# Optimization experiments

Hardware: AMD Instinct MI355X
Metric: run time of the kernel (lower is better)

## Reference

```python
import jax, jax.numpy as jnp
import numpy as np

EPS = 1e-5
LEAK = 0.1
NPOINT = 4096
NSAMPLE = 32


def setup_inputs() -> dict:
    key = jax.random.key(0)
    ks = jax.random.split(key, 6)
    B, N, Cin = 2, 16384, 64
    ch = [Cin + 3, 64, 64, 128]
    xyz = jax.random.normal(ks[0], (B, 3, N), jnp.float32)
    points = jax.random.normal(ks[1], (B, Cin, N), jnp.float32)
    W0 = jax.random.normal(ks[2], (ch[1], ch[0]), jnp.float32) * 0.05
    W1 = jax.random.normal(ks[3], (ch[2], ch[1]), jnp.float32) * 0.05
    W2 = jax.random.normal(ks[4], (ch[3], ch[2]), jnp.float32) * 0.05
    return dict(
        xyz=xyz, points=points, W0=W0, W1=W1, W2=W2,
        g0=jnp.ones((ch[1],), jnp.float32), b0=jnp.zeros((ch[1],), jnp.float32),
        g1=jnp.ones((ch[2],), jnp.float32), b1=jnp.zeros((ch[2],), jnp.float32),
        g2=jnp.ones((ch[3],), jnp.float32), b2=jnp.zeros((ch[3],), jnp.float32),
    )


def _mlp_bn_act(x, W, g, b):
    # 1x1 conv (no bias) + BatchNorm2d (training: batch stats, biased var) + LeakyReLU(0.1)
    x = jnp.einsum('oc,bcsk->bosk', W, x)
    m = jnp.mean(x, axis=(0, 2, 3), keepdims=True)
    v = jnp.mean(jnp.square(x - m), axis=(0, 2, 3), keepdims=True)
    x = (x - m) * jax.lax.rsqrt(v + EPS) * g[None, :, None, None] + b[None, :, None, None]
    return jnp.where(x >= 0, x, LEAK * x)


def reference(xyz, points, W0, W1, W2, g0, b0, g1, b1, g2, b2):
    B, _, N = xyz.shape
    xyz_t = jnp.transpose(xyz, (0, 2, 1))            # [B,N,3]
    new_xyz = xyz[:, :, :NPOINT]                     # [B,3,S]  (use_fps=False path)
    new_xyz_t = jnp.transpose(new_xyz, (0, 2, 1))    # [B,S,3]

    # squared distances [B,S,N]
    d = (jnp.sum(new_xyz_t ** 2, -1)[:, :, None]
         + jnp.sum(xyz_t ** 2, -1)[:, None, :]
         - 2.0 * jnp.einsum('bsc,bnc->bsn', new_xyz_t, xyz_t))
    _, knn_idx = jax.lax.top_k(-d, NSAMPLE)          # [B,S,K] nearest neighbors

    gather = jax.vmap(lambda arr, idx: arr[idx])     # ([N,C],[S,K]) -> [S,K,C]
    neighbor_xyz = gather(xyz_t, knn_idx)            # [B,S,K,3]
    direction = neighbor_xyz - new_xyz_t[:, :, None, :]
    grouped = gather(jnp.transpose(points, (0, 2, 1)), knn_idx)  # [B,S,K,Cin]

    x = jnp.transpose(jnp.concatenate([direction, grouped], -1), (0, 3, 1, 2))  # [B,Cin+3,S,K]
    x = _mlp_bn_act(x, W0, g0, b0)
    x = _mlp_bn_act(x, W1, g1, b1)
    x = _mlp_bn_act(x, W2, g2, b2)
    new_points = jnp.max(x, axis=-1)                 # [B,128,S] max-pool over nsample
    return new_xyz, new_points
```

## Files before the change

### kernel.cpp

```cpp
#include <hip/hip_runtime.h>
#include <hip/hip_bf16.h>
#include <stdint.h>

#define N_ALL   16384
#define NPOINT  4096
#define KNN_K   32
#define BATCH   2
#define P_TOT   (BATCH*NPOINT*KNN_K)
#define P_TOTF  262144.0f
#define EPSV    1e-5f

typedef __attribute__((ext_vector_type(8))) short bf16x8;
typedef __attribute__((ext_vector_type(4))) float f32x4;

__device__ unsigned short g_knn[P_TOT];
__device__ __attribute__((aligned(16))) float g_pxyzn[BATCH*N_ALL*4];
__device__ __attribute__((aligned(16))) short g_ptb[BATCH*N_ALL*64];
__device__ __attribute__((aligned(16))) short g_x0b[(size_t)P_TOT*64];
__device__ __attribute__((aligned(16))) short g_x1b[(size_t)P_TOT*64];
__device__ __attribute__((aligned(16))) short g_x2b[(size_t)P_TOT*128];
__device__ __attribute__((aligned(16))) short g_Wb0[4*3*64*8];
__device__ __attribute__((aligned(16))) short g_Wb1[4*2*64*8];
__device__ __attribute__((aligned(16))) short g_Wb2[8*2*64*8];
__device__ float g_part0[128], g_part1[128], g_part2[256];

__device__ __forceinline__ float b2f(short s) {
  union { unsigned u; float f; } v; v.u = ((unsigned)(unsigned short)s) << 16; return v.f;
}
__device__ __forceinline__ short f2b(float f) {
  union { float f; unsigned u; } v; v.f = f;
  unsigned u = v.u;
  u += 0x7FFFu + ((u >> 16) & 1u);
  return (short)(u >> 16);
}
__device__ __forceinline__ unsigned pkbf(float a, float b) {
  union { __hip_bfloat162 h; unsigned u; } v;
  v.h = __float22bfloat162_rn(make_float2(a, b));
  return v.u;
}
__device__ __forceinline__ unsigned long long bperm64(unsigned long long v, int byteaddr) {
  int lo = __builtin_amdgcn_ds_bpermute(byteaddr, (int)(unsigned)(v & 0xFFFFFFFFULL));
  int hi = __builtin_amdgcn_ds_bpermute(byteaddr, (int)(unsigned)(v >> 32));
  return (((unsigned long long)(unsigned)hi) << 32) | (unsigned)lo;
}
__device__ __forceinline__ unsigned long long u64min(unsigned long long a, unsigned long long b) {
  return a < b ? a : b;
}
__device__ __forceinline__ unsigned long long selstage(unsigned long long v,
                                                       unsigned long long pv, bool mx) {
  bool lt = v < pv;
  return (lt != mx) ? v : pv;
}

__device__ __forceinline__ void knn_merge32(unsigned long long& vL,
                                            unsigned long long& worst,
                                            unsigned& worst_hi, float& wd,
                                            unsigned long long vB, int hl,
                                            int aX1, int aX2, int aX4, int aX8,
                                            int aX16, int aRev, int aW) {
  vB = selstage(vB, bperm64(vB, aX1),  ((hl & 1) != 0) != ((hl & 2) != 0));
  vB = selstage(vB, bperm64(vB, aX2),  ((hl & 2) != 0) != ((hl & 4) != 0));
  vB = selstage(vB, bperm64(vB, aX1),  ((hl & 1) != 0) != ((hl & 4) != 0));
  vB = selstage(vB, bperm64(vB, aX4),  ((hl & 4) != 0) != ((hl & 8) != 0));
  vB = selstage(vB, bperm64(vB, aX2),  ((hl & 2) != 0) != ((hl & 8) != 0));
  vB = selstage(vB, bperm64(vB, aX1),  ((hl & 1) != 0) != ((hl & 8) != 0));
  vB = selstage(vB, bperm64(vB, aX8),  ((hl & 8) != 0) != ((hl & 16) != 0));
  vB = selstage(vB, bperm64(vB, aX4),  ((hl & 4) != 0) != ((hl & 16) != 0));
  vB = selstage(vB, bperm64(vB, aX2),  ((hl & 2) != 0) != ((hl & 16) != 0));
  vB = selstage(vB, bperm64(vB, aX1),  ((hl & 1) != 0) != ((hl & 16) != 0));
  vB = selstage(vB, bperm64(vB, aX16), (hl & 16) != 0);
  vB = selstage(vB, bperm64(vB, aX8),  (hl & 8) != 0);
  vB = selstage(vB, bperm64(vB, aX4),  (hl & 4) != 0);
  vB = selstage(vB, bperm64(vB, aX2),  (hl & 2) != 0);
  vB = selstage(vB, bperm64(vB, aX1),  (hl & 1) != 0);
  vL = u64min(vL, bperm64(vB, aRev));
  vL = selstage(vL, bperm64(vL, aX16), (hl & 16) != 0);
  vL = selstage(vL, bperm64(vL, aX8),  (hl & 8) != 0);
  vL = selstage(vL, bperm64(vL, aX4),  (hl & 4) != 0);
  vL = selstage(vL, bperm64(vL, aX2),  (hl & 2) != 0);
  vL = selstage(vL, bperm64(vL, aX1),  (hl & 1) != 0);
  worst = bperm64(vL, aW);
  worst_hi = (unsigned)(worst >> 32);
  unsigned wh = worst_hi;
  unsigned ub = (wh & 0x80000000u) ? (wh ^ 0x80000000u) : ~wh;
  wd = (wh == 0xFFFFFFFFu) ? __builtin_inff() : __uint_as_float(ub);
}

__global__ __launch_bounds__(256) void k_setup(const float* __restrict__ xyz,
                                               const float* __restrict__ points,
                                               const float* __restrict__ W0,
                                               const float* __restrict__ W1,
                                               const float* __restrict__ W2,
                                               float* __restrict__ out) {
#pragma clang fp contract(off)
  __shared__ float tile[64][65];
  int blk = blockIdx.x;
  int t = threadIdx.x;
  if (blk < 512) {
    int b  = blk >> 8;
    int n0 = (blk & 255) << 6;
#pragma unroll
    for (int r = 0; r < 16; r++) {
      int lin = r * 256 + t;
      int c = lin >> 6, nn = lin & 63;
      tile[c][nn] = points[((size_t)(b * 64 + c)) * N_ALL + n0 + nn];
    }
    __syncthreads();
#pragma unroll
    for (int r = 0; r < 16; r++) {
      int lin = r * 256 + t;
      int nn = lin >> 6, c = lin & 63;
      g_ptb[((size_t)(b * N_ALL + n0 + nn)) * 64 + c] = f2b(tile[c][nn]);
    }
  } else if (blk < 640) {
    int i = (blk - 512) * 256 + t;
    if (i < 24576) {
      int s = i & 4095;
      int c = (i >> 12) % 3;
      int b = i / 12288;
      out[i] = xyz[(b * 3 + c) * N_ALL + s];
    }
    int b = i >> 14, n = i & 16383;
    const float* xb = xyz + b * 3 * N_ALL;
    float x = xb[n], y = xb[N_ALL + n], z = xb[2 * N_ALL + n];
    float4 p; p.x = x; p.y = y; p.z = z; p.w = x * x + y * y + z * z;
    ((float4*)g_pxyzn)[i] = p;
  } else {
    for (int i = t; i < 4 * 3 * 64 * 8; i += 256) {
      int j = i & 7, lane = (i >> 3) & 63, rest = i >> 9;
      int kt = rest % 3, mt = rest / 3;
      int m = 16 * mt + (lane & 15);
      int k = 32 * kt + (lane >> 4) * 8 + j;
      float v = 0.f;
      if (k < 64) v = W0[m * 67 + 3 + k];
      else if (k < 67) v = W0[m * 67 + (k - 64)];
      g_Wb0[i] = f2b(v);
    }
    for (int i = t; i < 4 * 2 * 64 * 8; i += 256) {
      int j = i & 7, lane = (i >> 3) & 63;
      int kt = (i >> 9) & 1, mt = i >> 10;
      int m = 16 * mt + (lane & 15);
      int k = 32 * kt + (lane >> 4) * 8 + j;
      g_Wb1[i] = f2b(W1[m * 64 + k]);
    }
    for (int i = t; i < 8 * 2 * 64 * 8; i += 256) {
      int j = i & 7, lane = (i >> 3) & 63;
      int kt = (i >> 9) & 1, mt = i >> 10;
      int m = 16 * mt + (lane & 15);
      int k = 32 * kt + (lane >> 4) * 8 + j;
      g_Wb2[i] = f2b(W2[m * 64 + k]);
    }
    if (t < 128) { g_part0[t] = 0.f; g_part1[t] = 0.f; }
    g_part2[t] = 0.f;
  }
}

__global__ __launch_bounds__(256, 8) void k_knn() {
#pragma clang fp contract(off)
  __shared__ unsigned long long buf[4][2][64];
  int wv = threadIdx.x >> 6;
  int lane = threadIdx.x & 63;
  int half = lane >> 5;
  int hl = lane & 31;
  int lanebase = lane & 32;
  unsigned long long* bufh = buf[wv][half];

  int qpair = wv >> 1;
  int range = wv & 1;
  int q = blockIdx.x * 4 + qpair * 2 + half;
  int b = q >> 12, s = q & 4095;
  const float4* pb = (const float4*)g_pxyzn + (b << 14);
  float4 qp = pb[s];
  float qx = qp.x, qy = qp.y, qz = qp.z, qn = qp.w;

  int aX1  = (lanebase | (hl ^ 1))  << 2;
  int aX2  = (lanebase | (hl ^ 2))  << 2;
  int aX4  = (lanebase | (hl ^ 4))  << 2;
  int aX8  = (lanebase | (hl ^ 8))  << 2;
  int aX16 = (lanebase | (hl ^ 16)) << 2;
  int aRev = (lanebase | (31 - hl)) << 2;
  int aW   = (lanebase | 31)        << 2;

  unsigned long long vL = ~0ULL;
  unsigned long long worst = ~0ULL;
  unsigned worst_hi = 0xFFFFFFFFu;
  float wd = __builtin_inff();
  int F = 0;

  int base = range << 13;
  for (int n0 = base; n0 < base + 8192; n0 += 128) {
    float4 p0 = pb[n0 + hl];
    float4 p1 = pb[n0 + 32 + hl];
    float4 p2 = pb[n0 + 64 + hl];
    float4 p3 = pb[n0 + 96 + hl];
    float d[4];
    {
      float dt0 = (qx * p0.x + qy * p0.y) + qz * p0.z;
      float dt1 = (qx * p1.x + qy * p1.y) + qz * p1.z;
      float dt2 = (qx * p2.x + qy * p2.y) + qz * p2.z;
      float dt3 = (qx * p3.x + qy * p3.y) + qz * p3.z;
      d[0] = __builtin_fmaf(-2.0f, dt0, qn + p0.w);
      d[1] = __builtin_fmaf(-2.0f, dt1, qn + p1.w);
      d[2] = __builtin_fmaf(-2.0f, dt2, qn + p2.w);
      d[3] = __builtin_fmaf(-2.0f, dt3, qn + p3.w);
    }
    float md = fminf(fminf(d[0], d[1]), fminf(d[2], d[3]));
    if (__ballot(md <= wd)) {
#pragma unroll
      for (int t = 0; t < 4; t++) {
        bool sv = d[t] <= wd;
        unsigned long long bl = __ballot(sv);
        unsigned mb = half ? (unsigned)(bl >> 32) : (unsigned)bl;
        if (sv) {
          unsigned u = __float_as_uint(d[t]);
          u ^= ((unsigned)(((int)u) >> 31)) | 0x80000000u;
          unsigned long long c = (((unsigned long long)u) << 32)
                               | (unsigned)(n0 + 32 * t + hl);
          bufh[F + __popc(mb & ((1u << hl) - 1u))] = c;
        }
        F += __popc(mb);
        if (__ballot(F >= 32)) {
          int take = F >= 32 ? 32 : F;
          unsigned long long vB = (hl < take) ? bufh[hl] : ~0ULL;
          knn_merge32(vL, worst, worst_hi, wd, vB, hl,
                      aX1, aX2, aX4, aX8, aX16, aRev, aW);
          int R = F - take;
          if (hl < R) bufh[hl] = bufh[32 + hl];
          F = R;
        }
      }
    }
  }
  if (__ballot(F > 0)) {
    unsigned long long vB = (hl < F) ? bufh[hl] : ~0ULL;
    knn_merge32(vL, worst, worst_hi, wd, vB, hl, aX1, aX2, aX4, aX8, aX16, aRev, aW);
  }

  bufh[hl] = vL;
  __syncthreads();
  unsigned long long vB = buf[wv ^ 1][half][hl];
  vL = u64min(vL, bperm64(vB, aRev));
  vL = selstage(vL, bperm64(vL, aX16), (hl & 16) != 0);
  vL = selstage(vL, bperm64(vL, aX8),  (hl & 8) != 0);
  vL = selstage(vL, bperm64(vL, aX4),  (hl & 4) != 0);
  vL = selstage(vL, bperm64(vL, aX2),  (hl & 2) != 0);
  vL = selstage(vL, bperm64(vL, aX1),  (hl & 1) != 0);
  if (range == 0)
    g_knn[((size_t)q << 5) | hl] = (unsigned short)(vL & 0xFFFF);
}

__global__ __launch_bounds__(256) void k_l0(const float* __restrict__ xyz) {
  __shared__ short feats[256][104];
  int t = threadIdx.x;
  int p0 = blockIdx.x * 256;
  {
    int p = p0 + t;
    int idx = g_knn[p];
    int s = (p >> 5) & 4095;
    int b = p >> 17;
    const short* src = g_ptb + ((size_t)((b << 14) + idx) << 6);
#pragma unroll
    for (int i = 0; i < 8; i++)
      ((int4*)&feats[t][0])[i] = ((const int4*)src)[i];
    const float* xb = xyz + b * 3 * N_ALL;
    feats[t][64] = f2b(xb[idx] - xb[s]);
    feats[t][65] = f2b(xb[N_ALL + idx] - xb[N_ALL + s]);
    feats[t][66] = f2b(xb[2 * N_ALL + idx] - xb[2 * N_ALL + s]);
#pragma unroll
    for (int c = 67; c < 96; c++) feats[t][c] = 0;
  }
  __syncthreads();
  int lane = t & 63, wv = t >> 6;
  int l15 = lane & 15, quad = lane >> 4;
  bf16x8 A[4][3];
#pragma unroll
  for (int mt = 0; mt < 4; mt++)
#pragma unroll
    for (int kt = 0; kt < 3; kt++)
      A[mt][kt] = *(const bf16x8*)(g_Wb0 + (((mt * 3 + kt) * 64 + lane) << 3));
  f32x4 C[4][4];
#pragma unroll
  for (int mt = 0; mt < 4; mt++)
#pragma unroll
    for (int nt = 0; nt < 4; nt++) C[mt][nt] = 0.f;
#pragma unroll
  for (int kt = 0; kt < 3; kt++)
#pragma unroll
    for (int nt = 0; nt < 4; nt++) {
      bf16x8 B = *(const bf16x8*)(&feats[wv * 64 + nt * 16 + l15][kt * 32 + quad * 8]);
#pragma unroll
      for (int mt = 0; mt < 4; mt++)
        C[mt][nt] = __builtin_amdgcn_mfma_f32_16x16x32_bf16(A[mt][kt], B, C[mt][nt], 0, 0, 0);
    }
#pragma unroll
  for (int mt = 0; mt < 4; mt++)
#pragma unroll
    for (int nt = 0; nt < 4; nt++) {
      int p = p0 + wv * 64 + nt * 16 + l15;
      int c0 = mt * 16 + quad * 4;
      uint2 o;
      o.x = pkbf(C[mt][nt][0], C[mt][nt][1]);
      o.y = pkbf(C[mt][nt][2], C[mt][nt][3]);
      *(uint2*)(g_x0b + ((size_t)p << 6) + c0) = o;
    }
}

__global__ __launch_bounds__(256) void k_l1(const float* __restrict__ g0,
                                            const float* __restrict__ b0) {
  __shared__ float scA[64], shA[64];
  int t = threadIdx.x;
  if (t < 64) {
    float m = g_part0[t] / P_TOTF;
    float v = g_part0[64 + t] / P_TOTF - m * m;
    float sc = g0[t] / sqrtf(v + EPSV);
    scA[t] = sc; shA[t] = b0[t] - m * sc;
  }
  __syncthreads();
  int lane = t & 63, wv = t >> 6;
  int l15 = lane & 15, quad = lane >> 4;
  int p0 = blockIdx.x * 256 + wv * 64;
  float scv[2][8], shv[2][8];
#pragma unroll
  for (int kt = 0; kt < 2; kt++)
#pragma unroll
    for (int j = 0; j < 8; j++) {
      int c = kt * 32 + quad * 8 + j;
      scv[kt][j] = scA[c]; shv[kt][j] = shA[c];
    }
  bf16x8 A[4][2];
#pragma unroll
  for (int mt = 0; mt < 4; mt++)
#pragma unroll
    for (int kt = 0; kt < 2; kt++)
      A[mt][kt] = *(const bf16x8*)(g_Wb1 + (((mt * 2 + kt) * 64 + lane) << 3));
  f32x4 C[4][4];
#pragma unroll
  for (int mt = 0; mt < 4; mt++)
#pragma unroll
    for (int nt = 0; nt < 4; nt++) C[mt][nt] = 0.f;
#pragma unroll
  for (int kt = 0; kt < 2; kt++)
#pragma unroll
    for (int nt = 0; nt < 4; nt++) {
      const short* src = g_x0b + (((size_t)(p0 + nt * 16 + l15)) << 6) + kt * 32 + quad * 8;
      uint4 raw = *(const uint4*)src;
      bf16x8 B;
      unsigned* Bu = (unsigned*)&B;
      unsigned ru[4] = {raw.x, raw.y, raw.z, raw.w};
#pragma unroll
      for (int jj = 0; jj < 4; jj++) {
        float lo = __uint_as_float(ru[jj] << 16);
        float hi = __uint_as_float(ru[jj] & 0xFFFF0000u);
        float a0 = lo * scv[kt][2*jj]   + shv[kt][2*jj];
        float a1 = hi * scv[kt][2*jj+1] + shv[kt][2*jj+1];
        a0 = fmaxf(a0, 0.1f * a0);
        a1 = fmaxf(a1, 0.1f * a1);
        Bu[jj] = pkbf(a0, a1);
      }
#pragma unroll
      for (int mt = 0; mt < 4; mt++)
        C[mt][nt] = __builtin_amdgcn_mfma_f32_16x16x32_bf16(A[mt][kt], B, C[mt][nt], 0, 0, 0);
    }
#pragma unroll
  for (int mt = 0; mt < 4; mt++)
#pragma unroll
    for (int nt = 0; nt < 4; nt++) {
      int p = p0 + nt * 16 + l15;
      int c0 = mt * 16 + quad * 4;
      uint2 o;
      o.x = pkbf(C[mt][nt][0], C[mt][nt][1]);
      o.y = pkbf(C[mt][nt][2], C[mt][nt][3]);
      *(uint2*)(g_x1b + ((size_t)p << 6) + c0) = o;
    }
}

__global__ __launch_bounds__(256) void k_l2(const float* __restrict__ g1,
                                            const float* __restrict__ b1) {
  __shared__ float scA[64], shA[64];
  int t = threadIdx.x;
  if (t < 64) {
    float m = g_part1[t] / P_TOTF;
    float v = g_part1[64 + t] / P_TOTF - m * m;
    float sc = g1[t] / sqrtf(v + EPSV);
    scA[t] = sc; shA[t] = b1[t] - m * sc;
  }
  __syncthreads();
  int lane = t & 63, wv = t >> 6;
  int l15 = lane & 15, quad = lane >> 4;
  int chh = wv & 1;
  int p0 = blockIdx.x * 128 + (wv >> 1) * 64;
  float scv[2][8], shv[2][8];
#pragma unroll
  for (int kt = 0; kt < 2; kt++)
#pragma unroll
    for (int j = 0; j < 8; j++) {
      int c = kt * 32 + quad * 8 + j;
      scv[kt][j] = scA[c]; shv[kt][j] = shA[c];
    }
  bf16x8 A[4][2];
#pragma unroll
  for (int mt = 0; mt < 4; mt++)
#pragma unroll
    for (int kt = 0; kt < 2; kt++)
      A[mt][kt] = *(const bf16x8*)(g_Wb2 + ((((4 * chh + mt) * 2 + kt) * 64 + lane) << 3));
  f32x4 C[4][4];
#pragma unroll
  for (int mt = 0; mt < 4; mt++)
#pragma unroll
    for (int nt = 0; nt < 4; nt++) C[mt][nt] = 0.f;
#pragma unroll
  for (int kt = 0; kt < 2; kt++)
#pragma unroll
    for (int nt = 0; nt < 4; nt++) {
      const short* src = g_x1b + (((size_t)(p0 + nt * 16 + l15)) << 6) + kt * 32 + quad * 8;
      uint4 raw = *(const uint4*)src;
      bf16x8 B;
      unsigned* Bu = (unsigned*)&B;
      unsigned ru[4] = {raw.x, raw.y, raw.z, raw.w};
#pragma unroll
      for (int jj = 0; jj < 4; jj++) {
        float lo = __uint_as_float(ru[jj] << 16);
        float hi = __uint_as_float(ru[jj] & 0xFFFF0000u);
        float a0 = lo * scv[kt][2*jj]   + shv[kt][2*jj];
        float a1 = hi * scv[kt][2*jj+1] + shv[kt][2*jj+1];
        a0 = fmaxf(a0, 0.1f * a0);
        a1 = fmaxf(a1, 0.1f * a1);
        Bu[jj] = pkbf(a0, a1);
      }
#pragma unroll
      for (int mt = 0; mt < 4; mt++)
        C[mt][nt] = __builtin_amdgcn_mfma_f32_16x16x32_bf16(A[mt][kt], B, C[mt][nt], 0, 0, 0);
    }
#pragma unroll
  for (int mt = 0; mt < 4; mt++)
#pragma unroll
    for (int nt = 0; nt < 4; nt++) {
      int p = p0 + nt * 16 + l15;
      int c0 = (4 * chh + mt) * 16 + quad * 4;
      uint2 o;
      o.x = pkbf(C[mt][nt][0], C[mt][nt][1]);
      o.y = pkbf(C[mt][nt][2], C[mt][nt][3]);
      *(uint2*)(g_x2b + ((size_t)p << 7) + c0) = o;
    }
}

__global__ __launch_bounds__(256) void k_red64(const short* __restrict__ x,
                                               float* __restrict__ part) {
  int t = threadIdx.x;
  int cl = t & 31, pr = t >> 5;
  float s0 = 0.f, s1 = 0.f, q0 = 0.f, q1 = 0.f;
  int pbase = blockIdx.x * 1024;
  for (int i = 0; i < 128; i++) {
    int p = pbase + pr + i * 8;
    unsigned d = *(const unsigned*)(x + ((size_t)p << 6) + cl * 2);
    float a = b2f((short)(d & 0xFFFF));
    float b = b2f((short)(d >> 16));
    s0 += a; q0 = fmaf(a, a, q0);
    s1 += b; q1 = fmaf(b, b, q1);
  }
  __shared__ float sm[8][64], sq[8][64];
  sm[pr][cl * 2] = s0; sm[pr][cl * 2 + 1] = s1;
  sq[pr][cl * 2] = q0; sq[pr][cl * 2 + 1] = q1;
  __syncthreads();
  if (t < 64) {
    float S = 0.f, Q = 0.f;
#pragma unroll
    for (int r = 0; r < 8; r++) { S += sm[r][t]; Q += sq[r][t]; }
    atomicAdd(part + t, S); atomicAdd(part + 64 + t, Q);
  }
}

__global__ __launch_bounds__(256) void k_red128(const short* __restrict__ x,
                                                float* __restrict__ part) {
  int t = threadIdx.x;
  int cl = t & 63, pr = t >> 6;
  float s0 = 0.f, s1 = 0.f, q0 = 0.f, q1 = 0.f;
  int pbase = blockIdx.x * 1024;
  for (int i = 0; i < 256; i++) {
    int p = pbase + pr + i * 4;
    unsigned d = *(const unsigned*)(x + ((size_t)p << 7) + cl * 2);
    float a = b2f((short)(d & 0xFFFF));
    float b = b2f((short)(d >> 16));
    s0 += a; q0 = fmaf(a, a, q0);
    s1 += b; q1 = fmaf(b, b, q1);
  }
  __shared__ float sm[4][128], sq[4][128];
  sm[pr][cl * 2] = s0; sm[pr][cl * 2 + 1] = s1;
  sq[pr][cl * 2] = q0; sq[pr][cl * 2 + 1] = q1;
  __syncthreads();
  if (t < 128) {
    float S = 0.f, Q = 0.f;
#pragma unroll
    for (int r = 0; r < 4; r++) { S += sm[r][t]; Q += sq[r][t]; }
    atomicAdd(part + t, S); atomicAdd(part + 128 + t, Q);
  }
}

__global__ __launch_bounds__(256) void k_epi(const float* __restrict__ g2,
                                             const float* __restrict__ b2,
                                             float* __restrict__ out) {
  __shared__ float scA[128], shA[128];
  __shared__ float res[16][132];
  int t = threadIdx.x;
  if (t < 128) {
    float m = g_part2[t] / P_TOTF;
    float v = g_part2[128 + t] / P_TOTF - m * m;
    float sc = g2[t] / sqrtf(v + EPSV);
    scA[t] = sc; shA[t] = b2[t] - m * sc;
  }
  __syncthreads();
  int cp = t & 63, sl = t >> 6;
  int c0 = cp * 2, c1 = c0 + 1;
  float sc0 = scA[c0], sh0 = shA[c0];
  float sc1 = scA[c1], sh1 = shA[c1];
  int sg0 = blockIdx.x * 16;
  for (int it = 0; it < 4; it++) {
    int sgl = sl * 4 + it;
    size_t pbase = ((size_t)(sg0 + sgl)) << 5;
    float mx0 = -3.4e38f, mn0 = 3.4e38f, mx1 = -3.4e38f, mn1 = 3.4e38f;
#pragma unroll
    for (int k = 0; k < 32; k++) {
      unsigned u = *(const unsigned*)(g_x2b + ((pbase + k) << 7) + cp * 2);
      float v0 = __uint_as_float(u << 16);
      float v1 = __uint_as_float(u & 0xFFFF0000u);
      mx0 = fmaxf(mx0, v0); mn0 = fminf(mn0, v0);
      mx1 = fmaxf(mx1, v1); mn1 = fminf(mn1, v1);
    }
    float a0 = (sc0 >= 0.f ? mx0 : mn0) * sc0 + sh0; a0 = fmaxf(a0, 0.1f * a0);
    float a1 = (sc1 >= 0.f ? mx1 : mn1) * sc1 + sh1; a1 = fmaxf(a1, 0.1f * a1);
    res[sgl][c0] = a0; res[sgl][c1] = a1;
  }
  __syncthreads();
  int b = sg0 >> 12, s0 = sg0 & 4095;
#pragma unroll
  for (int w = 0; w < 2; w++) {
    int fidx = t * 2 + w;
    int c = fidx >> 2, qi = fidx & 3;
    float4 o;
    o.x = res[qi * 4 + 0][c];
    o.y = res[qi * 4 + 1][c];
    o.z = res[qi * 4 + 2][c];
    o.w = res[qi * 4 + 3][c];
    *(float4*)(out + 24576 + (((size_t)(b * 128 + c)) << 12) + s0 + qi * 4) = o;
  }
}

extern "C" void kernel_launch(void* const* d_in, const int* in_sizes, int n_in,
                              void* d_out, int out_size, void* d_ws, size_t ws_size,
                              hipStream_t stream) {
  (void)in_sizes; (void)n_in; (void)out_size; (void)d_ws; (void)ws_size;
  const float* xyz    = (const float*)d_in[0];
  const float* points = (const float*)d_in[1];
  const float* W0     = (const float*)d_in[2];
  const float* W1     = (const float*)d_in[3];
  const float* W2     = (const float*)d_in[4];
  const float* g0     = (const float*)d_in[5];
  const float* b0     = (const float*)d_in[6];
  const float* g1     = (const float*)d_in[7];
  const float* b1     = (const float*)d_in[8];
  const float* g2     = (const float*)d_in[9];
  const float* b2     = (const float*)d_in[10];
  float* out = (float*)d_out;

  short *x0b, *x1b, *x2b; float *part0, *part1, *part2;
  hipGetSymbolAddress((void**)&x0b,   HIP_SYMBOL(g_x0b));
  hipGetSymbolAddress((void**)&x1b,   HIP_SYMBOL(g_x1b));
  hipGetSymbolAddress((void**)&x2b,   HIP_SYMBOL(g_x2b));
  hipGetSymbolAddress((void**)&part0, HIP_SYMBOL(g_part0));
  hipGetSymbolAddress((void**)&part1, HIP_SYMBOL(g_part1));
  hipGetSymbolAddress((void**)&part2, HIP_SYMBOL(g_part2));

  hipLaunchKernelGGL(k_setup,  dim3(641),  dim3(256), 0, stream, xyz, points, W0, W1, W2, out);
  hipLaunchKernelGGL(k_knn,    dim3(2048), dim3(256), 0, stream);
  hipLaunchKernelGGL(k_l0,     dim3(1024), dim3(256), 0, stream, xyz);
  hipLaunchKernelGGL(k_red64,  dim3(256),  dim3(256), 0, stream, x0b, part0);
  hipLaunchKernelGGL(k_l1,     dim3(1024), dim3(256), 0, stream, g0, b0);
  hipLaunchKernelGGL(k_red64,  dim3(256),  dim3(256), 0, stream, x1b, part1);
  hipLaunchKernelGGL(k_l2,     dim3(2048), dim3(256), 0, stream, g1, b1);
  hipLaunchKernelGGL(k_red128, dim3(256),  dim3(256), 0, stream, x2b, part2);
  hipLaunchKernelGGL(k_epi,    dim3(512),  dim3(256), 0, stream, g2, b2, out);
}
```

Measured before the change: 321.5 us.

## Fuse per-group max/min pooling into layer-2 stats reduction, vectorize feature padding

The final BN-statistics reduction now walks points group by group and also computes each group's per-channel max and min, writing them to small float buffers. The epilogue then reads these precomputed extrema instead of re-reading the full 128-channel bf16 activation tensor. This removes a second full pass over the largest intermediate, in exchange for small extra buffers and a changed access order in the reduction. Separately, the zero padding and direction features in k_l0 are written with vector stores instead of scalar ones.

```diff
diff --git a/kernel.cpp b/kernel.cpp
--- a/kernel.cpp
+++ b/kernel.cpp
@@ -19,6 +19,8 @@
 __device__ __attribute__((aligned(16))) short g_x0b[(size_t)P_TOT*64];
 __device__ __attribute__((aligned(16))) short g_x1b[(size_t)P_TOT*64];
 __device__ __attribute__((aligned(16))) short g_x2b[(size_t)P_TOT*128];
+__device__ __attribute__((aligned(16))) float g_mx[(size_t)BATCH*NPOINT*128];
+__device__ __attribute__((aligned(16))) float g_mn[(size_t)BATCH*NPOINT*128];
 __device__ __attribute__((aligned(16))) short g_Wb0[4*3*64*8];
 __device__ __attribute__((aligned(16))) short g_Wb1[4*2*64*8];
 __device__ __attribute__((aligned(16))) short g_Wb2[8*2*64*8];
@@ -263,11 +265,17 @@
     for (int i = 0; i < 8; i++)
       ((int4*)&feats[t][0])[i] = ((const int4*)src)[i];
     const float* xb = xyz + b * 3 * N_ALL;
-    feats[t][64] = f2b(xb[idx] - xb[s]);
-    feats[t][65] = f2b(xb[N_ALL + idx] - xb[N_ALL + s]);
-    feats[t][66] = f2b(xb[2 * N_ALL + idx] - xb[2 * N_ALL + s]);
-#pragma unroll
-    for (int c = 67; c < 96; c++) feats[t][c] = 0;
+    int4 z; z.x = 0; z.y = 0; z.z = 0; z.w = 0;
+    *(int4*)&feats[t][64] = z;
+    *(int4*)&feats[t][72] = z;
+    *(int4*)&feats[t][80] = z;
+    *(int4*)&feats[t][88] = z;
+    short4 d3;
+    d3.x = f2b(xb[idx] - xb[s]);
+    d3.y = f2b(xb[N_ALL + idx] - xb[N_ALL + s]);
+    d3.z = f2b(xb[2 * N_ALL + idx] - xb[2 * N_ALL + s]);
+    d3.w = 0;
+    *(short4*)&feats[t][64] = d3;
   }
   __syncthreads();
   int lane = t & 63, wv = t >> 6;
@@ -470,23 +478,34 @@
   }
 }
 
-__global__ __launch_bounds__(256) void k_red128(const short* __restrict__ x,
-                                                float* __restrict__ part) {
-  int t = threadIdx.x;
-  int cl = t & 63, pr = t >> 6;
+__global__ __launch_bounds__(256) void k_red128mx(const short* __restrict__ x,
+                                                  float* __restrict__ part) {
+  int t = threadIdx.x;
+  int cl = t & 63, wv = t >> 6;
   float s0 = 0.f, s1 = 0.f, q0 = 0.f, q1 = 0.f;
-  int pbase = blockIdx.x * 1024;
-  for (int i = 0; i < 256; i++) {
-    int p = pbase + pr + i * 4;
-    unsigned d = *(const unsigned*)(x + ((size_t)p << 7) + cl * 2);
-    float a = b2f((short)(d & 0xFFFF));
-    float b = b2f((short)(d >> 16));
-    s0 += a; q0 = fmaf(a, a, q0);
-    s1 += b; q1 = fmaf(b, b, q1);
+  int g0 = blockIdx.x * 32;
+  for (int it = 0; it < 8; it++) {
+    int g = g0 + it * 4 + wv;
+    size_t pbase = (size_t)g << 5;
+    float mx0 = -3.4e38f, mn0 = 3.4e38f, mx1 = -3.4e38f, mn1 = 3.4e38f;
+#pragma unroll
+    for (int k = 0; k < 32; k++) {
+      unsigned d = *(const unsigned*)(x + ((pbase + k) << 7) + cl * 2);
+      float a = __uint_as_float(d << 16);
+      float b = __uint_as_float(d & 0xFFFF0000u);
+      s0 += a; q0 = fmaf(a, a, q0);
+      s1 += b; q1 = fmaf(b, b, q1);
+      mx0 = fmaxf(mx0, a); mn0 = fminf(mn0, a);
+      mx1 = fmaxf(mx1, b); mn1 = fminf(mn1, b);
+    }
+    float2 vmx; vmx.x = mx0; vmx.y = mx1;
+    float2 vmn; vmn.x = mn0; vmn.y = mn1;
+    *(float2*)(g_mx + ((size_t)g << 7) + cl * 2) = vmx;
+    *(float2*)(g_mn + ((size_t)g << 7) + cl * 2) = vmn;
   }
   __shared__ float sm[4][128], sq[4][128];
-  sm[pr][cl * 2] = s0; sm[pr][cl * 2 + 1] = s1;
-  sq[pr][cl * 2] = q0; sq[pr][cl * 2 + 1] = q1;
+  sm[wv][cl * 2] = s0; sm[wv][cl * 2 + 1] = s1;
+  sq[wv][cl * 2] = q0; sq[wv][cl * 2 + 1] = q1;
   __syncthreads();
   if (t < 128) {
     float S = 0.f, Q = 0.f;
@@ -516,18 +535,11 @@
   int sg0 = blockIdx.x * 16;
   for (int it = 0; it < 4; it++) {
     int sgl = sl * 4 + it;
-    size_t pbase = ((size_t)(sg0 + sgl)) << 5;
-    float mx0 = -3.4e38f, mn0 = 3.4e38f, mx1 = -3.4e38f, mn1 = 3.4e38f;
-#pragma unroll
-    for (int k = 0; k < 32; k++) {
-      unsigned u = *(const unsigned*)(g_x2b + ((pbase + k) << 7) + cp * 2);
-      float v0 = __uint_as_float(u << 16);
-      float v1 = __uint_as_float(u & 0xFFFF0000u);
-      mx0 = fmaxf(mx0, v0); mn0 = fminf(mn0, v0);
-      mx1 = fmaxf(mx1, v1); mn1 = fminf(mn1, v1);
-    }
-    float a0 = (sc0 >= 0.f ? mx0 : mn0) * sc0 + sh0; a0 = fmaxf(a0, 0.1f * a0);
-    float a1 = (sc1 >= 0.f ? mx1 : mn1) * sc1 + sh1; a1 = fmaxf(a1, 0.1f * a1);
+    size_t off = ((size_t)(sg0 + sgl) << 7) + c0;
+    float2 vmx = *(const float2*)(g_mx + off);
+    float2 vmn = *(const float2*)(g_mn + off);
+    float a0 = (sc0 >= 0.f ? vmx.x : vmn.x) * sc0 + sh0; a0 = fmaxf(a0, 0.1f * a0);
+    float a1 = (sc1 >= 0.f ? vmx.y : vmn.y) * sc1 + sh1; a1 = fmaxf(a1, 0.1f * a1);
     res[sgl][c0] = a0; res[sgl][c1] = a1;
   }
   __syncthreads();
@@ -570,13 +582,13 @@
   hipGetSymbolAddress((void**)&part1, HIP_SYMBOL(g_part1));
   hipGetSymbolAddress((void**)&part2, HIP_SYMBOL(g_part2));
 
-  hipLaunchKernelGGL(k_setup,  dim3(641),  dim3(256), 0, stream, xyz, points, W0, W1, W2, out);
-  hipLaunchKernelGGL(k_knn,    dim3(2048), dim3(256), 0, stream);
-  hipLaunchKernelGGL(k_l0,     dim3(1024), dim3(256), 0, stream, xyz);
-  hipLaunchKernelGGL(k_red64,  dim3(256),  dim3(256), 0, stream, x0b, part0);
-  hipLaunchKernelGGL(k_l1,     dim3(1024), dim3(256), 0, stream, g0, b0);
-  hipLaunchKernelGGL(k_red64,  dim3(256),  dim3(256), 0, stream, x1b, part1);
-  hipLaunchKernelGGL(k_l2,     dim3(2048), dim3(256), 0, stream, g1, b1);
-  hipLaunchKernelGGL(k_red128, dim3(256),  dim3(256), 0, stream, x2b, part2);
-  hipLaunchKernelGGL(k_epi,    dim3(512),  dim3(256), 0, stream, g2, b2, out);
-}
+  hipLaunchKernelGGL(k_setup,    dim3(641),  dim3(256), 0, stream, xyz, points, W0, W1, W2, out);
+  hipLaunchKernelGGL(k_knn,      dim3(2048), dim3(256), 0, stream);
+  hipLaunchKernelGGL(k_l0,       dim3(1024), dim3(256), 0, stream, xyz);
+  hipLaunchKernelGGL(k_red64,    dim3(256),  dim3(256), 0, stream, x0b, part0);
+  hipLaunchKernelGGL(k_l1,       dim3(1024), dim3(256), 0, stream, g0, b0);
+  hipLaunchKernelGGL(k_red64,    dim3(256),  dim3(256), 0, stream, x1b, part1);
+  hipLaunchKernelGGL(k_l2,       dim3(2048), dim3(256), 0, stream, g1, b1);
+  hipLaunchKernelGGL(k_red128mx, dim3(256),  dim3(256), 0, stream, x2b, part2);
+  hipLaunchKernelGGL(k_epi,      dim3(512),  dim3(256), 0, stream, g2, b2, out);
+}
```

After: 312.1 us. 2.9% less time.
